# Optimization experiments

Measured on AMD Instinct MI355X. Metric: run time of the kernel, lower is better.

Reference implementation:

```python
import jax, jax.numpy as jnp
import numpy as np

EPS = 1e-5

def _bn(x, gamma, beta):
    # BatchNorm1d training-mode math: batch mean / biased variance over edge dim
    mean = jnp.mean(x, axis=0)
    var = jnp.mean(jnp.square(x - mean), axis=0)
    return (x - mean) * (gamma / jnp.sqrt(var + EPS)) + beta


def setup_inputs() -> dict:
    key = jax.random.key(0)
    ks = jax.random.split(key, 12)
    n, d, s, h, e = 50000, 256, 32, 128, 500000
    feat = 3 * d + s + 1  # 801
    sc = lambda fan_in: 1.0 / np.sqrt(fan_in)
    return {
        "node_embeddings": jax.random.normal(ks[0], (n, d), jnp.float32),
        "gradient_scores": jax.random.normal(ks[1], (e,), jnp.float32),
        "step_embedding": jax.random.normal(ks[2], (s,), jnp.float32),
        "W1": jax.random.normal(ks[3], (feat, h), jnp.float32) * sc(feat),
        "b1": jnp.zeros((h,), jnp.float32),
        "g1": jnp.ones((h,), jnp.float32),
        "be1": jnp.zeros((h,), jnp.float32),
        "W2": jax.random.normal(ks[4], (h, h // 2), jnp.float32) * sc(h),
        "b2": jnp.zeros((h // 2,), jnp.float32),
        "g2": jnp.ones((h // 2,), jnp.float32),
        "be2": jnp.zeros((h // 2,), jnp.float32),
        "W3": jax.random.normal(ks[5], (h // 2, 1), jnp.float32) * sc(h // 2),
        "b3": jnp.zeros((1,), jnp.float32),
        "edge_index": jax.random.randint(ks[6], (2, e), 0, n, jnp.int64),
    }


def reference(node_embeddings, gradient_scores, step_embedding,
              W1, b1, g1, be1, W2, b2, g2, be2, W3, b3, edge_index):
    src, dst = edge_index[0], edge_index[1]
    h_u = node_embeddings[src]              # [E, d]
    h_v = node_embeddings[dst]              # [E, d]
    edge_diff = jnp.abs(h_u - h_v)          # [E, d]
    E = edge_index.shape[1]
    step = jnp.broadcast_to(step_embedding[None, :], (E, step_embedding.shape[0]))
    feats = jnp.concatenate([h_u, h_v, edge_diff, step, gradient_scores[:, None]], axis=1)
    x = jnp.maximum(feats @ W1 + b1, 0.0)
    x = _bn(x, g1, be1)                     # dropout is identity in eval
    x = jnp.maximum(x @ W2 + b2, 0.0)
    x = _bn(x, g2, be2)
    out = jnp.tanh(x @ W3 + b3)[:, 0]       # [E]
    return out
```

## Files before the change

### kernel.cpp

```cpp
#include <hip/hip_runtime.h>

#define NE 500000
#define DIMK 256
#define H1 128
#define H2 64
#define EPSBN 1e-5f
#define GRID1 512
#define NT1 1954
#define GRID2 1024
#define NT2 3907

typedef _Float16 half8 __attribute__((ext_vector_type(8)));
typedef float f32x4 __attribute__((ext_vector_type(4)));
typedef unsigned short ushort8 __attribute__((ext_vector_type(8)));

typedef const __attribute__((address_space(1))) void* gas1_t;
typedef __attribute__((address_space(3))) void* las3_t;

static __device__ __forceinline__ half8 habs8(half8 x) {
  ushort8 u = __builtin_bit_cast(ushort8, x);
  u &= (unsigned short)0x7FFF;
  return __builtin_bit_cast(half8, u);
}
static __device__ __forceinline__ float h2f(unsigned int u) {
  return (float)__builtin_bit_cast(_Float16, (unsigned short)(u & 0xffff));
}
static __device__ __forceinline__ void gload_lds16(const _Float16* src, _Float16* dst) {
  __builtin_amdgcn_global_load_lds((gas1_t)src, (las3_t)dst, 16, 0, 0);
}

__global__ void k_prep(const float* __restrict__ W1, const float* __restrict__ b1,
                       const float* __restrict__ step, float* __restrict__ c0) {
  const int j = threadIdx.x;
  if (j < H1) {
    float a = b1[j];
#pragma unroll
    for (int tt = 0; tt < 32; ++tt) a += step[tt] * W1[(768 + tt) * H1 + j];
    c0[j] = a;
  }
}

__global__ void k_prep16(const float* __restrict__ emb, _Float16* __restrict__ embh) {
  const int i = (blockIdx.x * 256 + threadIdx.x) * 8;
  const float4 a = *(const float4*)(emb + i);
  const float4 b = *(const float4*)(emb + i + 4);
  half8 h;
  h[0] = (_Float16)a.x; h[1] = (_Float16)a.y; h[2] = (_Float16)a.z; h[3] = (_Float16)a.w;
  h[4] = (_Float16)b.x; h[5] = (_Float16)b.y; h[6] = (_Float16)b.z; h[7] = (_Float16)b.w;
  *(half8*)(embh + i) = h;
}

__global__ void k_prepB(const float* __restrict__ W1, _Float16* __restrict__ bfrag) {
  const int g = blockIdx.x * 256 + threadIdx.x;
  const int lane = g & 63, f = g >> 6;
  const int c = f & 7, kc = (f >> 3) & 7, s = f >> 6;
  const int row0 = s * 256 + kc * 32 + (lane >> 4) * 8;
  const int col = c * 16 + (lane & 15);
  half8 h;
#pragma unroll
  for (int j = 0; j < 8; ++j) h[j] = (_Float16)W1[(row0 + j) * H1 + col];
  *(half8*)(bfrag + (size_t)g * 8) = h;
}

#define STAGE1(q, kcv) do {                                                   \
    _Pragma("unroll")                                                         \
    for (int jj = 0; jj < 6; ++jj) {                                          \
      const int sc = jj * 4 + w;                                              \
      const int ff = (sc >> 3) * 64 + (kcv) * 8 + (sc & 7);                   \
      gload_lds16(bfrag + ((size_t)ff * 64 + lane) * 8,                       \
                  s_B + (size_t)(q) * 12288 + sc * 512);                      \
    }                                                                         \
  } while (0)

__global__ __launch_bounds__(256, 2)
void k_layer1(const _Float16* __restrict__ embh, const void* __restrict__ eidx_raw,
              const float* __restrict__ grad, const float* __restrict__ W1,
              const float* __restrict__ c0, const _Float16* __restrict__ bfrag,
              _Float16* __restrict__ x1, float* __restrict__ p1) {
  __shared__ int s_src[256], s_dst[256];
  __shared__ float s_g[256];
  __shared__ float s_wg[128], s_c0[128], s_sum[128], s_sq[128];
  __shared__ __align__(16) _Float16 s_B[2 * 12288];

  const int t = threadIdx.x, bid = blockIdx.x;
  const int w = t >> 6, lane = t & 63, quad = lane >> 4, m15 = lane & 15;

  if (t < 128) {
    s_wg[t] = W1[800 * H1 + t];
    s_c0[t] = c0[t];
    s_sum[t] = 0.f; s_sq[t] = 0.f;
  }

  const unsigned* ew = (const unsigned*)eidx_raw;
  const bool is64 = ((ew[1] | ew[3] | ew[5] | ew[7]) == 0u);
  const int* e32 = (const int*)eidx_raw;
  const long long* e64 = (const long long*)eidx_raw;

  float st_s[8] = {0, 0, 0, 0, 0, 0, 0, 0}, st_q[8] = {0, 0, 0, 0, 0, 0, 0, 0};

  for (int tile = bid; tile < NT1; tile += GRID1) {
    const int base = tile * 256;
    __syncthreads();
    {
      int e = base + t; if (e >= NE) e = NE - 1;
      if (is64) { s_src[t] = (int)e64[e]; s_dst[t] = (int)e64[NE + e]; }
      else      { s_src[t] = e32[e];      s_dst[t] = e32[NE + e]; }
      s_g[t] = grad[e];
    }
    STAGE1(0, 0);
    __syncthreads();

    const int r0 = w * 64 + m15;
    const _Float16* pu[4];
    const _Float16* pv[4];
#pragma unroll
    for (int r = 0; r < 4; ++r) {
      pu[r] = embh + (size_t)s_src[r0 + r * 16] * DIMK + quad * 8;
      pv[r] = embh + (size_t)s_dst[r0 + r * 16] * DIMK + quad * 8;
    }
    f32x4 acc[4][8];
#pragma unroll
    for (int r = 0; r < 4; ++r)
#pragma unroll
      for (int c = 0; c < 8; ++c) acc[r][c] = (f32x4)0.f;

#pragma unroll 1
    for (int kc = 0; kc < 8; ++kc) {
      if (kc < 7) {
        STAGE1((kc + 1) & 1, kc + 1);
        asm volatile("s_waitcnt vmcnt(6)" ::: "memory");
      } else {
        asm volatile("s_waitcnt vmcnt(0)" ::: "memory");
      }
      __builtin_amdgcn_s_barrier();
      __builtin_amdgcn_sched_barrier(0);

      half8 u[4], v[4], d[4];
#pragma unroll
      for (int r = 0; r < 4; ++r) {
        u[r] = *(const half8*)(pu[r] + kc * 32);
        v[r] = *(const half8*)(pv[r] + kc * 32);
      }
#pragma unroll
      for (int r = 0; r < 4; ++r) d[r] = habs8(u[r] - v[r]);

      const half8* bq = (const half8*)s_B + (size_t)(kc & 1) * 1536 + lane;
#pragma unroll
      for (int c = 0; c < 8; ++c) {
        const half8 bu = bq[c * 64];
        const half8 bv = bq[512 + c * 64];
        const half8 bd = bq[1024 + c * 64];
#pragma unroll
        for (int r = 0; r < 4; ++r)
          acc[r][c] = __builtin_amdgcn_mfma_f32_16x16x32_f16(u[r], bu, acc[r][c], 0, 0, 0);
#pragma unroll
        for (int r = 0; r < 4; ++r)
          acc[r][c] = __builtin_amdgcn_mfma_f32_16x16x32_f16(v[r], bv, acc[r][c], 0, 0, 0);
#pragma unroll
        for (int r = 0; r < 4; ++r)
          acc[r][c] = __builtin_amdgcn_mfma_f32_16x16x32_f16(d[r], bd, acc[r][c], 0, 0, 0);
      }
      __builtin_amdgcn_sched_barrier(0);
      __builtin_amdgcn_s_barrier();
    }
#pragma unroll
    for (int r = 0; r < 4; ++r) {
      const int erow = w * 64 + r * 16 + quad * 4;
#pragma unroll
      for (int c = 0; c < 8; ++c) {
        const int colL = c * 16 + m15;
        const float wgv = s_wg[colL], c0v = s_c0[colL];
#pragma unroll
        for (int reg = 0; reg < 4; ++reg) {
          const int e = base + erow + reg;
          float x = acc[r][c][reg] + s_g[erow + reg] * wgv + c0v;
          x = fmaxf(x, 0.f);
          if (e >= NE) x = 0.f;
          st_s[c] += x; st_q[c] += x * x;
          if (e < NE) x1[(size_t)e * H1 + colL] = (_Float16)x;
        }
      }
    }
  }
  __syncthreads();
#pragma unroll
  for (int c = 0; c < 8; ++c) {
    float a = st_s[c]; a += __shfl_xor(a, 16); a += __shfl_xor(a, 32);
    float b = st_q[c]; b += __shfl_xor(b, 16); b += __shfl_xor(b, 32);
    if (lane < 16) { atomicAdd(&s_sum[c * 16 + m15], a); atomicAdd(&s_sq[c * 16 + m15], b); }
  }
  __syncthreads();
  if (t < 128) {
    p1[t * GRID1 + bid] = s_sum[t];
    p1[128 * GRID1 + t * GRID1 + bid] = s_sq[t];
  }
}

__global__ void k_fin1(const float* __restrict__ p1, const float* __restrict__ g1,
                       const float* __restrict__ be1, const float* __restrict__ W2,
                       const float* __restrict__ b2, float* __restrict__ w2f,
                       float* __restrict__ b2f) {
  __shared__ float s1[128], t1[128];
  const int t = threadIdx.x;
  if (t < 128) {
    float s = 0.f, q = 0.f;
    const float4* rs = (const float4*)(p1 + t * GRID1);
    const float4* rq = (const float4*)(p1 + 128 * GRID1 + t * GRID1);
#pragma unroll 4
    for (int i = 0; i < GRID1 / 4; ++i) {
      float4 a = rs[i]; s += a.x + a.y + a.z + a.w;
      float4 b = rq[i]; q += b.x + b.y + b.z + b.w;
    }
    const float inv = 1.0f / (float)NE;
    float mean = s * inv;
    float var = q * inv - mean * mean;
    float sc = g1[t] * rsqrtf(var + EPSBN);
    s1[t] = sc; t1[t] = be1[t] - mean * sc;
  }
  __syncthreads();
  for (int i = t; i < H1 * H2; i += 256) w2f[i] = s1[i >> 6] * W2[i];
  if (t < 64) {
    float b = b2[t];
    for (int j = 0; j < 128; ++j) b += t1[j] * W2[j * 64 + t];
    b2f[t] = b;
  }
}

__global__ __launch_bounds__(256, 4)
void k_layer2(const _Float16* __restrict__ x1, const float* __restrict__ w2f,
              const float* __restrict__ b2f, _Float16* __restrict__ x2,
              float* __restrict__ p2) {
  __shared__ __align__(16) _Float16 b_lds[8192];
  __shared__ float s_b[64], s_sum[64], s_sq[64];
  const int t = threadIdx.x, bid = blockIdx.x;
  const int w = t >> 6, lane = t & 63, quad = lane >> 4, m15 = lane & 15;
  const int rg = w >> 1, cg = w & 1;

  for (int i = t; i < 8192; i += 256) {
    const int j = i & 7, li = (i >> 3) & 63, f = i >> 9;
    const int c = f & 3, kk = f >> 2;
    const int row = kk * 32 + (li >> 4) * 8 + j;
    const int col = c * 16 + (li & 15);
    b_lds[i] = (_Float16)w2f[row * H2 + col];
  }
  if (t < 64) { s_b[t] = b2f[t]; s_sum[t] = 0.f; s_sq[t] = 0.f; }
  __syncthreads();

  float st_s[2] = {0, 0}, st_q[2] = {0, 0};
  const half8* bp = (const half8*)b_lds;

  for (int job = bid; job < NT2; job += GRID2) {
    const int base = job * 128;
    const _Float16* pa[4];
#pragma unroll
    for (int r = 0; r < 4; ++r) {
      int e = base + rg * 64 + r * 16 + m15; if (e >= NE) e = NE - 1;
      pa[r] = x1 + (size_t)e * H1 + quad * 8;
    }
    f32x4 acc[4][2];
#pragma unroll
    for (int r = 0; r < 4; ++r)
#pragma unroll
      for (int c = 0; c < 2; ++c) acc[r][c] = (f32x4)0.f;

#pragma unroll
    for (int kk = 0; kk < 4; ++kk) {
      half8 a[4];
#pragma unroll
      for (int r = 0; r < 4; ++r) a[r] = *(const half8*)(pa[r] + kk * 32);
#pragma unroll
      for (int c = 0; c < 2; ++c) {
        const half8 bf = bp[(kk * 4 + cg * 2 + c) * 64 + lane];
#pragma unroll
        for (int r = 0; r < 4; ++r)
          acc[r][c] = __builtin_amdgcn_mfma_f32_16x16x32_f16(a[r], bf, acc[r][c], 0, 0, 0);
      }
    }
#pragma unroll
    for (int r = 0; r < 4; ++r) {
      const int erow = rg * 64 + r * 16 + quad * 4;
#pragma unroll
      for (int c = 0; c < 2; ++c) {
        const int colL = cg * 32 + c * 16 + m15;
        const float bv = s_b[colL];
#pragma unroll
        for (int reg = 0; reg < 4; ++reg) {
          const int e = base + erow + reg;
          float x = acc[r][c][reg] + bv;
          x = fmaxf(x, 0.f);
          if (e >= NE) x = 0.f;
          st_s[c] += x; st_q[c] += x * x;
          if (e < NE) x2[(size_t)e * H2 + colL] = (_Float16)x;
        }
      }
    }
  }
  __syncthreads();
#pragma unroll
  for (int c = 0; c < 2; ++c) {
    float a = st_s[c]; a += __shfl_xor(a, 16); a += __shfl_xor(a, 32);
    float b = st_q[c]; b += __shfl_xor(b, 16); b += __shfl_xor(b, 32);
    if (lane < 16) {
      atomicAdd(&s_sum[cg * 32 + c * 16 + m15], a);
      atomicAdd(&s_sq[cg * 32 + c * 16 + m15], b);
    }
  }
  __syncthreads();
  if (t < 64) {
    p2[t * GRID2 + bid] = s_sum[t];
    p2[64 * GRID2 + t * GRID2 + bid] = s_sq[t];
  }
}

__global__ void k_fin2(const float* __restrict__ p2, const float* __restrict__ g2,
                       const float* __restrict__ be2, const float* __restrict__ W3,
                       const float* __restrict__ b3, float* __restrict__ w3f,
                       float* __restrict__ b3f) {
  __shared__ float tp[64];
  const int t = threadIdx.x;
  if (t < 64) {
    float s = 0.f, q = 0.f;
    const float4* rs = (const float4*)(p2 + t * GRID2);
    const float4* rq = (const float4*)(p2 + 64 * GRID2 + t * GRID2);
#pragma unroll 4
    for (int i = 0; i < GRID2 / 4; ++i) {
      float4 a = rs[i]; s += a.x + a.y + a.z + a.w;
      float4 b = rq[i]; q += b.x + b.y + b.z + b.w;
    }
    const float inv = 1.0f / (float)NE;
    float mean = s * inv;
    float var = q * inv - mean * mean;
    float sc = g2[t] * rsqrtf(var + EPSBN);
    float tt = be2[t] - mean * sc;
    w3f[t] = sc * W3[t];
    tp[t] = tt * W3[t];
  }
  __syncthreads();
  if (t == 0) {
    float b = b3[0];
    for (int j = 0; j < 64; ++j) b += tp[j];
    b3f[0] = b;
  }
}

__global__ __launch_bounds__(256)
void k_out(const unsigned short* __restrict__ x2, const float* __restrict__ w3f,
           const float* __restrict__ b3f, float* __restrict__ out) {
  __shared__ float s_w[64];
  __shared__ float s_b;
  const int t = threadIdx.x;
  if (t < 64) s_w[t] = w3f[t];
  if (t == 0) s_b = b3f[0];
  __syncthreads();
  const int gid = blockIdx.x * 256 + t;
  const int e = gid >> 2, p = gid & 3;
  if (e < NE) {
    const uint4* r = (const uint4*)(x2 + (size_t)e * H2 + p * 16);
    float s = 0.f;
#pragma unroll
    for (int i = 0; i < 2; ++i) {
      const uint4 u = r[i];
      const int jb = p * 16 + i * 8;
      s += h2f(u.x) * s_w[jb + 0] + h2f(u.x >> 16) * s_w[jb + 1];
      s += h2f(u.y) * s_w[jb + 2] + h2f(u.y >> 16) * s_w[jb + 3];
      s += h2f(u.z) * s_w[jb + 4] + h2f(u.z >> 16) * s_w[jb + 5];
      s += h2f(u.w) * s_w[jb + 6] + h2f(u.w >> 16) * s_w[jb + 7];
    }
    s += __shfl_xor(s, 1);
    s += __shfl_xor(s, 2);
    if (p == 0) out[e] = tanhf(s + s_b);
  }
}

extern "C" void kernel_launch(void* const* d_in, const int* in_sizes, int n_in,
                              void* d_out, int out_size, void* d_ws, size_t ws_size,
                              hipStream_t stream) {
  const float* emb  = (const float*)d_in[0];
  const float* grad = (const float*)d_in[1];
  const float* step = (const float*)d_in[2];
  const float* W1   = (const float*)d_in[3];
  const float* b1   = (const float*)d_in[4];
  const float* g1   = (const float*)d_in[5];
  const float* be1  = (const float*)d_in[6];
  const float* W2   = (const float*)d_in[7];
  const float* b2   = (const float*)d_in[8];
  const float* g2   = (const float*)d_in[9];
  const float* be2  = (const float*)d_in[10];
  const float* W3   = (const float*)d_in[11];
  const float* b3   = (const float*)d_in[12];
  const void*  eidx = (const void*)d_in[13];
  float* out = (float*)d_out;

  char* ws = (char*)d_ws;
  _Float16* embh  = (_Float16*)(ws + 0);
  _Float16* x2    = (_Float16*)(ws + 0);
  _Float16* bfrag = (_Float16*)(ws + 25600000LL);
  float*    c0    = (float*)(ws + 25796608LL);
  float*    p1    = (float*)(ws + 26000000LL);
  _Float16* x1    = (_Float16*)(ws + 64000000LL);
  float* p2  = (float*)(ws + 192000000LL);
  float* w2f = (float*)(ws + 192524288LL);
  float* b2f = (float*)(ws + 192557056LL);
  float* w3f = (float*)(ws + 192557312LL);
  float* b3f = (float*)(ws + 192557568LL);

  k_prep  <<<1,    256, 0, stream>>>(W1, b1, step, c0);
  k_prep16<<<6250, 256, 0, stream>>>(emb, embh);
  k_prepB <<<48,   256, 0, stream>>>(W1, bfrag);
  k_layer1<<<GRID1,256, 0, stream>>>(embh, eidx, grad, W1, c0, bfrag, x1, p1);
  k_fin1  <<<1,    256, 0, stream>>>(p1, g1, be1, W2, b2, w2f, b2f);
  k_layer2<<<GRID2,256, 0, stream>>>(x1, w2f, b2f, x2, p2);
  k_fin2  <<<1,    128, 0, stream>>>(p2, g2, be2, W3, b3, w3f, b3f);
  k_out   <<<7813, 256, 0, stream>>>((const unsigned short*)x2, w3f, b3f, out);
}
```

Before: 366.4 us.

## Software-pipeline layer1 gathers and layer2 loads with smaller tiles and packed stores

```diff
diff --git a/kernel.cpp b/kernel.cpp
--- a/kernel.cpp
+++ b/kernel.cpp
@@ -5,10 +5,11 @@
 #define H1 128
 #define H2 64
 #define EPSBN 1e-5f
+#define TILE1 128
 #define GRID1 512
-#define NT1 1954
-#define GRID2 1024
-#define NT2 3907
+#define NT1 3907
+#define GRID2 512
+#define NJ2 1954
 
 typedef _Float16 half8 __attribute__((ext_vector_type(8)));
 typedef float f32x4 __attribute__((ext_vector_type(4)));
@@ -25,9 +26,17 @@
 static __device__ __forceinline__ float h2f(unsigned int u) {
   return (float)__builtin_bit_cast(_Float16, (unsigned short)(u & 0xffff));
 }
+static __device__ __forceinline__ unsigned packf16(float a, float b) {
+  unsigned lo = (unsigned)__builtin_bit_cast(unsigned short, (_Float16)a);
+  unsigned hi = (unsigned)__builtin_bit_cast(unsigned short, (_Float16)b);
+  return lo | (hi << 16);
+}
 static __device__ __forceinline__ void gload_lds16(const _Float16* src, _Float16* dst) {
   __builtin_amdgcn_global_load_lds((gas1_t)src, (las3_t)dst, 16, 0, 0);
 }
+
+#define WAITV(N) asm volatile("s_waitcnt vmcnt(" #N ")" ::: "memory")
+#define SB0 __builtin_amdgcn_sched_barrier(0)
 
 __global__ void k_prep(const float* __restrict__ W1, const float* __restrict__ b1,
                        const float* __restrict__ step, float* __restrict__ c0) {
@@ -72,24 +81,41 @@
     }                                                                         \
   } while (0)
 
+#define PREFA(pb, kcv) do {                                                   \
+    u[pb][0] = *(const half8*)(pu[0] + (kcv) * 32);                           \
+    u[pb][1] = *(const half8*)(pu[1] + (kcv) * 32);                           \
+    v[pb][0] = *(const half8*)(pv[0] + (kcv) * 32);                           \
+    v[pb][1] = *(const half8*)(pv[1] + (kcv) * 32);                           \
+  } while (0)
+
+#define MFMA_KC(pb) do {                                                      \
+    half8 d0 = habs8(u[pb][0] - v[pb][0]);                                    \
+    half8 d1 = habs8(u[pb][1] - v[pb][1]);                                    \
+    const half8* bq = (const half8*)s_B + (size_t)(pb) * 1536 + lane;         \
+    _Pragma("unroll")                                                         \
+    for (int c = 0; c < 8; ++c) {                                             \
+      half8 bu = bq[c * 64], bv = bq[512 + c * 64], bd = bq[1024 + c * 64];   \
+      acc[0][c] = __builtin_amdgcn_mfma_f32_16x16x32_f16(u[pb][0], bu, acc[0][c], 0, 0, 0); \
+      acc[1][c] = __builtin_amdgcn_mfma_f32_16x16x32_f16(u[pb][1], bu, acc[1][c], 0, 0, 0); \
+      acc[0][c] = __builtin_amdgcn_mfma_f32_16x16x32_f16(v[pb][0], bv, acc[0][c], 0, 0, 0); \
+      acc[1][c] = __builtin_amdgcn_mfma_f32_16x16x32_f16(v[pb][1], bv, acc[1][c], 0, 0, 0); \
+      acc[0][c] = __builtin_amdgcn_mfma_f32_16x16x32_f16(d0, bd, acc[0][c], 0, 0, 0); \
+      acc[1][c] = __builtin_amdgcn_mfma_f32_16x16x32_f16(d1, bd, acc[1][c], 0, 0, 0); \
+    }                                                                         \
+  } while (0)
+
 __global__ __launch_bounds__(256, 2)
 void k_layer1(const _Float16* __restrict__ embh, const void* __restrict__ eidx_raw,
               const float* __restrict__ grad, const float* __restrict__ W1,
               const float* __restrict__ c0, const _Float16* __restrict__ bfrag,
               _Float16* __restrict__ x1, float* __restrict__ p1) {
-  __shared__ int s_src[256], s_dst[256];
-  __shared__ float s_g[256];
-  __shared__ float s_wg[128], s_c0[128], s_sum[128], s_sq[128];
   __shared__ __align__(16) _Float16 s_B[2 * 12288];
+  __shared__ float s_sum[128], s_sq[128];
 
   const int t = threadIdx.x, bid = blockIdx.x;
   const int w = t >> 6, lane = t & 63, quad = lane >> 4, m15 = lane & 15;
 
-  if (t < 128) {
-    s_wg[t] = W1[800 * H1 + t];
-    s_c0[t] = c0[t];
-    s_sum[t] = 0.f; s_sq[t] = 0.f;
-  }
+  if (t < 128) { s_sum[t] = 0.f; s_sq[t] = 0.f; }
 
   const unsigned* ew = (const unsigned*)eidx_raw;
   const bool is64 = ((ew[1] | ew[3] | ew[5] | ew[7]) == 0u);
@@ -98,90 +124,120 @@
 
   float st_s[8] = {0, 0, 0, 0, 0, 0, 0, 0}, st_q[8] = {0, 0, 0, 0, 0, 0, 0, 0};
 
-  for (int tile = bid; tile < NT1; tile += GRID1) {
-    const int base = tile * 256;
-    __syncthreads();
-    {
-      int e = base + t; if (e >= NE) e = NE - 1;
-      if (is64) { s_src[t] = (int)e64[e]; s_dst[t] = (int)e64[NE + e]; }
-      else      { s_src[t] = e32[e];      s_dst[t] = e32[NE + e]; }
-      s_g[t] = grad[e];
-    }
-    STAGE1(0, 0);
-    __syncthreads();
-
-    const int r0 = w * 64 + m15;
-    const _Float16* pu[4];
-    const _Float16* pv[4];
-#pragma unroll
-    for (int r = 0; r < 4; ++r) {
-      pu[r] = embh + (size_t)s_src[r0 + r * 16] * DIMK + quad * 8;
-      pv[r] = embh + (size_t)s_dst[r0 + r * 16] * DIMK + quad * 8;
-    }
-    f32x4 acc[4][8];
-#pragma unroll
-    for (int r = 0; r < 4; ++r)
+  float wgr[8], c0r[8];
+#pragma unroll
+  for (int c = 0; c < 8; ++c) {
+    wgr[c] = W1[800 * H1 + c * 16 + m15];
+    c0r[c] = c0[c * 16 + m15];
+  }
+
+  int tile = bid;
+  int base = tile * TILE1;
+  const int r0 = w * 32 + m15;
+  int cs0, cs1, cd0, cd1;
+  {
+    int ea = base + r0;      if (ea >= NE) ea = NE - 1;
+    int eb = base + r0 + 16; if (eb >= NE) eb = NE - 1;
+    if (is64) { cs0 = (int)e64[ea]; cs1 = (int)e64[eb]; cd0 = (int)e64[NE + ea]; cd1 = (int)e64[NE + eb]; }
+    else      { cs0 = e32[ea];      cs1 = e32[eb];      cd0 = e32[NE + ea];      cd1 = e32[NE + eb]; }
+  }
+  WAITV(0); SB0;
+  const _Float16 *pu[2], *pv[2], *pun[2], *pvn[2];
+  pu[0] = embh + (size_t)cs0 * DIMK + quad * 8;
+  pu[1] = embh + (size_t)cs1 * DIMK + quad * 8;
+  pv[0] = embh + (size_t)cd0 * DIMK + quad * 8;
+  pv[1] = embh + (size_t)cd1 * DIMK + quad * 8;
+
+  half8 u[2][2], v[2][2];
+  f32x4 gr[2], grn[2];
+
+  STAGE1(0, 0);
+  PREFA(0, 0);
+  gr[0] = *(const f32x4*)(grad + base + w * 32 + quad * 4);
+  gr[1] = *(const f32x4*)(grad + base + w * 32 + 16 + quad * 4);
+
+  int n_s0 = 0, n_s1 = 0, n_d0 = 0, n_d1 = 0;
+
+  for (; tile < NT1; ) {
+    base = tile * TILE1;
+    const int bn = (tile + GRID1 < NT1) ? (tile + GRID1) * TILE1 : 0;
+
+    f32x4 acc[2][8];
+#pragma unroll
+    for (int r = 0; r < 2; ++r)
 #pragma unroll
       for (int c = 0; c < 8; ++c) acc[r][c] = (f32x4)0.f;
 
-#pragma unroll 1
+#pragma unroll
     for (int kc = 0; kc < 8; ++kc) {
-      if (kc < 7) {
-        STAGE1((kc + 1) & 1, kc + 1);
-        asm volatile("s_waitcnt vmcnt(6)" ::: "memory");
+      if (kc == 0)      WAITV(6);
+      else if (kc == 6) WAITV(8);
+      else              WAITV(4);
+      SB0;
+      __builtin_amdgcn_s_barrier();
+      SB0;
+      if (kc < 7) STAGE1((kc + 1) & 1, kc + 1);
+      else        STAGE1(0, 0);
+      WAITV(6);
+      SB0;
+      if (kc < 6) {
+        PREFA((kc + 1) & 1, kc + 1);
+        if (kc == 5) {
+          int ea = bn + r0;      if (ea >= NE) ea = NE - 1;
+          int eb = bn + r0 + 16; if (eb >= NE) eb = NE - 1;
+          if (is64) { n_s0 = (int)e64[ea]; n_s1 = (int)e64[eb]; n_d0 = (int)e64[NE + ea]; n_d1 = (int)e64[NE + eb]; }
+          else      { n_s0 = e32[ea];      n_s1 = e32[eb];      n_d0 = e32[NE + ea];      n_d1 = e32[NE + eb]; }
+        }
+      } else if (kc == 6) {
+        pun[0] = embh + (size_t)n_s0 * DIMK + quad * 8;
+        pun[1] = embh + (size_t)n_s1 * DIMK + quad * 8;
+        pvn[0] = embh + (size_t)n_d0 * DIMK + quad * 8;
+        pvn[1] = embh + (size_t)n_d1 * DIMK + quad * 8;
+        PREFA(1, 7);
       } else {
-        asm volatile("s_waitcnt vmcnt(0)" ::: "memory");
+        u[0][0] = *(const half8*)pun[0];
+        u[0][1] = *(const half8*)pun[1];
+        v[0][0] = *(const half8*)pvn[0];
+        v[0][1] = *(const half8*)pvn[1];
+        grn[0] = *(const f32x4*)(grad + bn + w * 32 + quad * 4);
+        grn[1] = *(const f32x4*)(grad + bn + w * 32 + 16 + quad * 4);
       }
-      __builtin_amdgcn_s_barrier();
-      __builtin_amdgcn_sched_barrier(0);
-
-      half8 u[4], v[4], d[4];
-#pragma unroll
-      for (int r = 0; r < 4; ++r) {
-        u[r] = *(const half8*)(pu[r] + kc * 32);
-        v[r] = *(const half8*)(pv[r] + kc * 32);
-      }
-#pragma unroll
-      for (int r = 0; r < 4; ++r) d[r] = habs8(u[r] - v[r]);
-
-      const half8* bq = (const half8*)s_B + (size_t)(kc & 1) * 1536 + lane;
+      MFMA_KC(kc & 1);
+    }
+
+#pragma unroll
+    for (int r = 0; r < 2; ++r) {
+      const int e0 = base + w * 32 + r * 16 + quad * 4;
 #pragma unroll
       for (int c = 0; c < 8; ++c) {
-        const half8 bu = bq[c * 64];
-        const half8 bv = bq[512 + c * 64];
-        const half8 bd = bq[1024 + c * 64];
-#pragma unroll
-        for (int r = 0; r < 4; ++r)
-          acc[r][c] = __builtin_amdgcn_mfma_f32_16x16x32_f16(u[r], bu, acc[r][c], 0, 0, 0);
-#pragma unroll
-        for (int r = 0; r < 4; ++r)
-          acc[r][c] = __builtin_amdgcn_mfma_f32_16x16x32_f16(v[r], bv, acc[r][c], 0, 0, 0);
-#pragma unroll
-        for (int r = 0; r < 4; ++r)
-          acc[r][c] = __builtin_amdgcn_mfma_f32_16x16x32_f16(d[r], bd, acc[r][c], 0, 0, 0);
-      }
-      __builtin_amdgcn_sched_barrier(0);
-      __builtin_amdgcn_s_barrier();
-    }
-#pragma unroll
-    for (int r = 0; r < 4; ++r) {
-      const int erow = w * 64 + r * 16 + quad * 4;
-#pragma unroll
-      for (int c = 0; c < 8; ++c) {
-        const int colL = c * 16 + m15;
-        const float wgv = s_wg[colL], c0v = s_c0[colL];
+        float xv[4];
 #pragma unroll
         for (int reg = 0; reg < 4; ++reg) {
-          const int e = base + erow + reg;
-          float x = acc[r][c][reg] + s_g[erow + reg] * wgv + c0v;
+          float x = acc[r][c][reg] + gr[r][reg] * wgr[c] + c0r[c];
           x = fmaxf(x, 0.f);
-          if (e >= NE) x = 0.f;
+          if (e0 + reg >= NE) x = 0.f;
+          xv[reg] = x;
           st_s[c] += x; st_q[c] += x * x;
-          if (e < NE) x1[(size_t)e * H1 + colL] = (_Float16)x;
+        }
+        unsigned b01 = packf16(xv[0], xv[1]);
+        unsigned b23 = packf16(xv[2], xv[3]);
+        unsigned q01 = (unsigned)__shfl_xor((int)b01, 1);
+        unsigned q23 = (unsigned)__shfl_xor((int)b23, 1);
+        const int ce = (c * 16 + m15) & ~1;
+        if (!(m15 & 1)) {
+          if (e0 < NE)     *(unsigned*)(x1 + (size_t)e0 * H1 + ce)       = (b01 & 0xffffu) | (q01 << 16);
+          if (e0 + 1 < NE) *(unsigned*)(x1 + (size_t)(e0 + 1) * H1 + ce) = (b01 >> 16) | (q01 & 0xffff0000u);
+        } else {
+          if (e0 + 2 < NE) *(unsigned*)(x1 + (size_t)(e0 + 2) * H1 + ce) = (q23 & 0xffffu) | (b23 << 16);
+          if (e0 + 3 < NE) *(unsigned*)(x1 + (size_t)(e0 + 3) * H1 + ce) = (q23 >> 16) | (b23 & 0xffff0000u);
         }
       }
     }
-  }
+    pu[0] = pun[0]; pu[1] = pun[1]; pv[0] = pvn[0]; pv[1] = pvn[1];
+    gr[0] = grn[0]; gr[1] = grn[1];
+    tile += GRID1;
+  }
+
   __syncthreads();
 #pragma unroll
   for (int c = 0; c < 8; ++c) {
@@ -226,7 +282,7 @@
   }
 }
 
-__global__ __launch_bounds__(256, 4)
+__global__ __launch_bounds__(256, 2)
 void k_layer2(const _Float16* __restrict__ x1, const float* __restrict__ w2f,
               const float* __restrict__ b2f, _Float16* __restrict__ x2,
               float* __restrict__ p2) {
@@ -234,7 +290,6 @@
   __shared__ float s_b[64], s_sum[64], s_sq[64];
   const int t = threadIdx.x, bid = blockIdx.x;
   const int w = t >> 6, lane = t & 63, quad = lane >> 4, m15 = lane & 15;
-  const int rg = w >> 1, cg = w & 1;
 
   for (int i = t; i < 8192; i += 256) {
     const int j = i & 7, li = (i >> 3) & 63, f = i >> 9;
@@ -246,64 +301,90 @@
   if (t < 64) { s_b[t] = b2f[t]; s_sum[t] = 0.f; s_sq[t] = 0.f; }
   __syncthreads();
 
-  float st_s[2] = {0, 0}, st_q[2] = {0, 0};
+  float bvr[4];
+#pragma unroll
+  for (int c = 0; c < 4; ++c) bvr[c] = s_b[c * 16 + m15];
+
+  float st_s[4] = {0, 0, 0, 0}, st_q[4] = {0, 0, 0, 0};
   const half8* bp = (const half8*)b_lds;
 
-  for (int job = bid; job < NT2; job += GRID2) {
-    const int base = job * 128;
-    const _Float16* pa[4];
-#pragma unroll
-    for (int r = 0; r < 4; ++r) {
-      int e = base + rg * 64 + r * 16 + m15; if (e >= NE) e = NE - 1;
-      pa[r] = x1 + (size_t)e * H1 + quad * 8;
-    }
-    f32x4 acc[4][2];
-#pragma unroll
-    for (int r = 0; r < 4; ++r)
-#pragma unroll
-      for (int c = 0; c < 2; ++c) acc[r][c] = (f32x4)0.f;
-
-#pragma unroll
-    for (int kk = 0; kk < 4; ++kk) {
-      half8 a[4];
-#pragma unroll
-      for (int r = 0; r < 4; ++r) a[r] = *(const half8*)(pa[r] + kk * 32);
-#pragma unroll
-      for (int c = 0; c < 2; ++c) {
-        const half8 bf = bp[(kk * 4 + cg * 2 + c) * 64 + lane];
-#pragma unroll
-        for (int r = 0; r < 4; ++r)
-          acc[r][c] = __builtin_amdgcn_mfma_f32_16x16x32_f16(a[r], bf, acc[r][c], 0, 0, 0);
-      }
-    }
-#pragma unroll
-    for (int r = 0; r < 4; ++r) {
-      const int erow = rg * 64 + r * 16 + quad * 4;
-#pragma unroll
-      for (int c = 0; c < 2; ++c) {
-        const int colL = cg * 32 + c * 16 + m15;
-        const float bv = s_b[colL];
-#pragma unroll
-        for (int reg = 0; reg < 4; ++reg) {
-          const int e = base + erow + reg;
-          float x = acc[r][c][reg] + bv;
-          x = fmaxf(x, 0.f);
-          if (e >= NE) x = 0.f;
-          st_s[c] += x; st_q[c] += x * x;
-          if (e < NE) x2[(size_t)e * H2 + colL] = (_Float16)x;
-        }
-      }
-    }
-  }
-  __syncthreads();
-#pragma unroll
-  for (int c = 0; c < 2; ++c) {
+  half8 a0[4][4], a1[4][4];
+
+#define L2LOAD(A, bb) do {                                                    \
+    _Pragma("unroll")                                                         \
+    for (int r = 0; r < 4; ++r) {                                             \
+      int e_ = (bb) + w * 64 + r * 16 + m15; if (e_ >= NE) e_ = NE - 1;       \
+      const _Float16* p_ = x1 + (size_t)e_ * H1 + quad * 8;                   \
+      _Pragma("unroll")                                                       \
+      for (int kk = 0; kk < 4; ++kk) (A)[kk][r] = *(const half8*)(p_ + kk * 32); \
+    } } while (0)
+
+#define L2COMP(A, bb) do {                                                    \
+    f32x4 acc[4][4];                                                          \
+    _Pragma("unroll")                                                         \
+    for (int r = 0; r < 4; ++r)                                               \
+      _Pragma("unroll")                                                       \
+      for (int c = 0; c < 4; ++c) acc[r][c] = (f32x4)0.f;                     \
+    _Pragma("unroll")                                                         \
+    for (int kk = 0; kk < 4; ++kk)                                            \
+      _Pragma("unroll")                                                       \
+      for (int c = 0; c < 4; ++c) {                                           \
+        half8 bf = bp[(kk * 4 + c) * 64 + lane];                              \
+        _Pragma("unroll")                                                     \
+        for (int r = 0; r < 4; ++r)                                           \
+          acc[r][c] = __builtin_amdgcn_mfma_f32_16x16x32_f16((A)[kk][r], bf, acc[r][c], 0, 0, 0); \
+      }                                                                       \
+    _Pragma("unroll")                                                         \
+    for (int r = 0; r < 4; ++r) {                                             \
+      const int e0 = (bb) + w * 64 + r * 16 + quad * 4;                       \
+      _Pragma("unroll")                                                       \
+      for (int c = 0; c < 4; ++c) {                                           \
+        float xv[4];                                                          \
+        _Pragma("unroll")                                                     \
+        for (int reg = 0; reg < 4; ++reg) {                                   \
+          float x = acc[r][c][reg] + bvr[c];                                  \
+          x = fmaxf(x, 0.f);                                                  \
+          if (e0 + reg >= NE) x = 0.f;                                        \
+          xv[reg] = x; st_s[c] += x; st_q[c] += x * x;                        \
+        }                                                                     \
+        unsigned b01 = packf16(xv[0], xv[1]);                                 \
+        unsigned b23 = packf16(xv[2], xv[3]);                                 \
+        unsigned q01 = (unsigned)__shfl_xor((int)b01, 1);                     \
+        unsigned q23 = (unsigned)__shfl_xor((int)b23, 1);                     \
+        const int ce = (c * 16 + m15) & ~1;                                   \
+        if (!(m15 & 1)) {                                                     \
+          if (e0 < NE)     *(unsigned*)(x2 + (size_t)e0 * H2 + ce)       = (b01 & 0xffffu) | (q01 << 16); \
+          if (e0 + 1 < NE) *(unsigned*)(x2 + (size_t)(e0 + 1) * H2 + ce) = (b01 >> 16) | (q01 & 0xffff0000u); \
+        } else {                                                              \
+          if (e0 + 2 < NE) *(unsigned*)(x2 + (size_t)(e0 + 2) * H2 + ce) = (q23 & 0xffffu) | (b23 << 16); \
+          if (e0 + 3 < NE) *(unsigned*)(x2 + (size_t)(e0 + 3) * H2 + ce) = (q23 >> 16) | (b23 & 0xffff0000u); \
+        }                                                                     \
+      }                                                                       \
+    } } while (0)
+
+  int j = bid;
+  if (j < NJ2) {
+    L2LOAD(a0, j * 256);
+    while (j < NJ2) {
+      const int j1 = j + GRID2;
+      L2LOAD(a1, (j1 < NJ2 ? j1 : j) * 256);
+      L2COMP(a0, j * 256);
+      if (j1 >= NJ2) break;
+      const int j2 = j1 + GRID2;
+      L2LOAD(a0, (j2 < NJ2 ? j2 : j1) * 256);
+      L2COMP(a1, j1 * 256);
+      j = j2;
+    }
+  }
+#undef L2LOAD
+#undef L2COMP
+
+  __syncthreads();
+#pragma unroll
+  for (int c = 0; c < 4; ++c) {
     float a = st_s[c]; a += __shfl_xor(a, 16); a += __shfl_xor(a, 32);
     float b = st_q[c]; b += __shfl_xor(b, 16); b += __shfl_xor(b, 32);
-    if (lane < 16) {
-      atomicAdd(&s_sum[cg * 32 + c * 16 + m15], a);
-      atomicAdd(&s_sq[cg * 32 + c * 16 + m15], b);
-    }
+    if (lane < 16) { atomicAdd(&s_sum[c * 16 + m15], a); atomicAdd(&s_sq[c * 16 + m15], b); }
   }
   __syncthreads();
   if (t < 64) {
```

New measurement: 426.4 us. +16.4%, slower.
